# Performance work log

Hardware: AMD Instinct MI355X
Metric: run time of the kernel (lower is better)

Reference implementation:

```python
import jax, jax.numpy as jnp
import numpy as np

N_NODES = 100000
N_EDGES = 1600000
IN_DIM = 3
HID = 128


def setup_inputs() -> dict:
    key = jax.random.key(0)
    ks = jax.random.split(key, 16)
    s = 0.05
    inp = {
        "x": jax.random.normal(ks[0], (N_NODES, IN_DIM), dtype=jnp.float32),
        "pos": jax.random.normal(ks[1], (N_NODES, IN_DIM), dtype=jnp.float32),
        "edge_index": jax.random.randint(ks[2], (2, N_EDGES), 0, N_NODES, dtype=jnp.int64),
        # EdgeConv MLP: Linear(2*IN_DIM, HID) -> ReLU -> Linear(HID, HID)
        "w1": jax.random.normal(ks[3], (2 * IN_DIM, HID), dtype=jnp.float32) * s,
        "b1": jnp.zeros((HID,), dtype=jnp.float32),
        "w2": jax.random.normal(ks[4], (HID, HID), dtype=jnp.float32) * s,
        "b2": jnp.zeros((HID,), dtype=jnp.float32),
        # encoder tail: ReLU -> Linear(HID, HID)
        "w3": jax.random.normal(ks[5], (HID, HID), dtype=jnp.float32) * s,
        "b3": jnp.zeros((HID,), dtype=jnp.float32),
        # decoder: Linear(HID, HID) -> ReLU -> Linear(HID, 3)
        "w4": jax.random.normal(ks[6], (HID, HID), dtype=jnp.float32) * s,
        "b4": jnp.zeros((HID,), dtype=jnp.float32),
        "w5": jax.random.normal(ks[7], (HID, 3), dtype=jnp.float32) * s,
        "b5": jnp.zeros((3,), dtype=jnp.float32),
    }
    return inp


def reference(x, pos, edge_index, w1, b1, w2, b2, w3, b3, w4, b4, w5, b5):
    n = x.shape[0]
    src, dst = edge_index[0], edge_index[1]  # message j(src) -> i(dst)
    xi = x[dst]                               # [E, 3] target features
    xj = x[src]                               # [E, 3] source features
    msg_in = jnp.concatenate([xi, xj - xi], axis=-1)          # [E, 6]
    h = jax.nn.relu(msg_in @ w1 + b1) @ w2 + b2               # [E, HID]
    agg = jax.ops.segment_max(h, dst, num_segments=n)         # [N, HID]
    agg = jnp.where(jnp.isneginf(agg), 0.0, agg)              # nodes with no edges -> 0
    enc = jax.nn.relu(agg) @ w3 + b3                          # [N, HID]
    dec = jax.nn.relu(enc @ w4 + b4) @ w5 + b5                # [N, 3]
    return pos + 0.1 * jnp.tanh(dec)
```

## Files before the change

kernel.cpp:

```cpp
#include <hip/hip_runtime.h>
#include <hip/hip_bf16.h>

typedef __attribute__((ext_vector_type(8))) short short8;
typedef __attribute__((ext_vector_type(4))) float floatx4;
typedef __attribute__((ext_vector_type(2))) unsigned short ushortx2;

#define NHID 128
#define PADROW 136
#define EB 64
#define EB2 128
#define PB 256

__device__ __forceinline__ unsigned short f2bf(float x) {
  unsigned int u = __float_as_uint(x);
  u += 0x7FFFu + ((u >> 16) & 1u);
  return (unsigned short)(u >> 16);
}

__device__ __forceinline__ unsigned int pkbf(float a, float b) {
  __hip_bfloat162 h = __float22bfloat162_rn(make_float2(a, b));
  union { __hip_bfloat162 h; unsigned int u; } cv;
  cv.h = h;
  return cv.u;
}

__device__ __forceinline__ unsigned int pack2(float a, float b) {
  return (unsigned int)f2bf(a) | ((unsigned int)f2bf(b) << 16);
}

__device__ __forceinline__ unsigned int pkmax(unsigned int a, unsigned int b) {
  union { unsigned int u; ushortx2 v; } x, y;
  x.u = a; y.u = b;
  x.v = __builtin_elementwise_max(x.v, y.v);
  return x.u;
}

__device__ __forceinline__ void casmax(unsigned int* ap, unsigned int run) {
  unsigned int old = *ap;
  while (true) {
    unsigned int mx = pkmax(old, run);
    if (mx == old) break;
    unsigned int got = atomicCAS(ap, old, mx);
    if (got == old) break;
    old = got;
  }
}

__device__ __forceinline__ void load_bfrags(const float* __restrict__ wmat,
                                            short8* bf, int m, int q) {
  #pragma unroll
  for (int kc = 0; kc < 4; ++kc) {
    #pragma unroll
    for (int nt = 0; nt < 8; ++nt) {
      short8 v;
      #pragma unroll
      for (int j = 0; j < 8; ++j)
        v[j] = (short)f2bf(wmat[(kc * 32 + q * 8 + j) * NHID + nt * 16 + m]);
      bf[kc * 8 + nt] = v;
    }
  }
}

__device__ __forceinline__ void load_bfrags_perm(const float* __restrict__ wmat,
                                                 short8* bf, int m, int q) {
  #pragma unroll
  for (int kc = 0; kc < 4; ++kc) {
    #pragma unroll
    for (int nt = 0; nt < 8; ++nt) {
      short8 v;
      #pragma unroll
      for (int j = 0; j < 8; ++j) {
        const int khw = kc * 32 + q * 8 + j;
        const int ctrue = ((khw & 7) << 4) | (khw >> 3);
        v[j] = (short)f2bf(wmat[ctrue * NHID + nt * 16 + m]);
      }
      bf[kc * 8 + nt] = v;
    }
  }
}

__device__ __forceinline__ void mfma_block(const unsigned short* uA,
                                           const short8* bf, floatx4* acc,
                                           int w, int m, int q) {
  #pragma unroll
  for (int kc = 0; kc < 4; ++kc) {
    short8 a = *(const short8*)(uA + (16 * w + m) * PADROW + kc * 32 + q * 8);
    #pragma unroll
    for (int nt = 0; nt < 8; ++nt)
      acc[nt] = __builtin_amdgcn_mfma_f32_16x16x32_bf16(a, bf[kc * 8 + nt],
                                                        acc[nt], 0, 0, 0);
  }
}

__global__ void zero_detect_kernel(float4* __restrict__ p, int n4,
                                   const int* __restrict__ ei, int* __restrict__ flag) {
  if (blockIdx.x == 0 && threadIdx.x < 64) {
    unsigned long long b = __ballot(ei[2 * threadIdx.x + 1] != 0);
    if (threadIdx.x == 0) flag[0] = (b == 0ULL) ? 1 : 0;
  }
  int i = blockIdx.x * blockDim.x + threadIdx.x;
  int stride = gridDim.x * blockDim.x;
  float4 z = make_float4(0.f, 0.f, 0.f, 0.f);
  for (; i < n4; i += stride) p[i] = z;
}


__global__ __launch_bounds__(256) void part_hist(const int* __restrict__ ei,
                                                 const int* __restrict__ flag,
                                                 int* __restrict__ mat, int E, int nbuck) {
  __shared__ int hist[512];
  const bool is64 = flag[0] != 0;
  const int bl = blockIdx.x, t = threadIdx.x;
  for (int i = t; i < nbuck; i += 256) hist[i] = 0;
  __syncthreads();
  const int chunk = (E + PB - 1) / PB;
  const int lo = bl * chunk;
  const int hi = min(lo + chunk, E);
  for (int i = lo + t; i < hi; i += 256) {
    int d = is64 ? ei[2 * E + 2 * i] : ei[E + i];
    atomicAdd(&hist[d >> 8], 1);
  }
  __syncthreads();
  for (int bu = t; bu < nbuck; bu += 256) mat[bu * PB + bl] = hist[bu];
}

__global__ __launch_bounds__(256) void scan_rows(int* __restrict__ mat,
                                                 int* __restrict__ btot, int nbuck) {
  __shared__ int sh[256];
  const int bu = blockIdx.x, t = threadIdx.x;
  const int v = mat[bu * PB + t];
  sh[t] = v;
  __syncthreads();
  for (int off = 1; off < 256; off <<= 1) {
    int x = (t >= off) ? sh[t - off] : 0;
    __syncthreads();
    sh[t] += x;
    __syncthreads();
  }
  mat[bu * PB + t] = sh[t] - v;
  if (t == 255) btot[bu] = sh[255];
}

__global__ __launch_bounds__(512) void scan_buckets(const int* __restrict__ btot,
                                                    int* __restrict__ bstart, int nbuck) {
  __shared__ int sh[512];
  const int t = threadIdx.x;
  const int v = (t < nbuck) ? btot[t] : 0;
  sh[t] = v;
  __syncthreads();
  for (int off = 1; off < 512; off <<= 1) {
    int x = (t >= off) ? sh[t - off] : 0;
    __syncthreads();
    sh[t] += x;
    __syncthreads();
  }
  if (t <= nbuck) bstart[t] = sh[t] - v;
}

__global__ __launch_bounds__(256) void part_scatter(const int* __restrict__ ei,
                                                    const int* __restrict__ flag,
                                                    const int* __restrict__ mat,
                                                    const int* __restrict__ bstart,
                                                    int2* __restrict__ mid, int E, int nbuck) {
  __shared__ int off[512];
  const bool is64 = flag[0] != 0;
  const int bl = blockIdx.x, t = threadIdx.x;
  for (int bu = t; bu < nbuck; bu += 256) off[bu] = bstart[bu] + mat[bu * PB + bl];
  __syncthreads();
  const int chunk = (E + PB - 1) / PB;
  const int lo = bl * chunk;
  const int hi = min(lo + chunk, E);
  for (int i = lo + t; i < hi; i += 256) {
    int s = is64 ? ei[2 * i]         : ei[i];
    int d = is64 ? ei[2 * E + 2 * i] : ei[E + i];
    int p = atomicAdd(&off[d >> 8], 1);
    mid[p] = make_int2(s, d);
  }
}

__global__ __launch_bounds__(256) void bucket_sort(const int2* __restrict__ mid,
                                                   const int* __restrict__ bstart,
                                                   int2* __restrict__ sorted) {
  __shared__ int h[256], cnt[256];
  const int bu = blockIdx.x, t = threadIdx.x;
  const int lo = bstart[bu], hi = bstart[bu + 1];
  h[t] = 0; cnt[t] = 0;
  __syncthreads();
  for (int i = lo + t; i < hi; i += 256) atomicAdd(&h[mid[i].y & 255], 1);
  __syncthreads();
  const int v = h[t];
  for (int off = 1; off < 256; off <<= 1) {
    int x = (t >= off) ? h[t - off] : 0;
    __syncthreads();
    h[t] += x;
    __syncthreads();
  }
  const int excl = h[t] - v;
  __syncthreads();
  h[t] = excl;
  __syncthreads();
  for (int i = lo + t; i < hi; i += 256) {
    int2 e = mid[i];
    const int dl = e.y & 255;
    const int p = lo + h[dl] + atomicAdd(&cnt[dl], 1);
    sorted[p] = e;
  }
}


__global__ __launch_bounds__(512, 2) void edge_sorted_kernel(
    const float* __restrict__ x, const int2* __restrict__ sorted,
    const float* __restrict__ w1, const float* __restrict__ b1,
    const float* __restrict__ w2, const float* __restrict__ b2,
    unsigned int* aggu, int N, int E) {
  __shared__ unsigned short us[EB2 * PADROW];
  __shared__ short8 w2f[2048];
  __shared__ int esS[EB2], edS[EB2];
  __shared__ int pn[2];
  __shared__ unsigned long long maskS[2];

  const int t = threadIdx.x;
  const int lane = t & 63;
  const int w = t >> 6;
  const int m = lane & 15;
  const int q = lane >> 4;

  float b1c[8], b2c[8];
  #pragma unroll
  for (int nt = 0; nt < 8; ++nt) { b1c[nt] = b1[nt * 16 + m]; b2c[nt] = b2[nt * 16 + m]; }

  short8 bf1[8];
  #pragma unroll
  for (int nt = 0; nt < 8; ++nt) {
    short8 v;
    #pragma unroll
    for (int j = 0; j < 8; ++j)
      v[j] = (q == 0 && j < 6) ? (short)f2bf(w1[j * NHID + nt * 16 + m]) : (short)0;
    bf1[nt] = v;
  }

  for (int idx = t; idx < 2048; idx += 512) {
    const int fg = idx >> 6, ln = idx & 63;
    const int mm = ln & 15;
    const int kc = fg >> 3, nt = fg & 7;
    short8 v;
    #pragma unroll
    for (int j = 0; j < 8; ++j) {
      const int khw = kc * 32 + (ln >> 4) * 8 + j;
      const int ctrue = ((khw & 7) << 4) | (khw >> 3);
      v[j] = (short)f2bf(w2[ctrue * NHID + nt * 16 + mm]);
    }
    w2f[idx] = v;
  }

  const int jc = t & 63;
  const int quarter = t >> 6;

  const int nbt = (E + EB2 - 1) / EB2;
  __syncthreads();

  int2 sv = make_int2(0, -1);
  {
    const int tile0 = blockIdx.x;
    const int gb = tile0 * EB2;
    if (t < EB2) {
      const int e = gb + t;
      if (tile0 < nbt && e < E) sv = sorted[e];
    } else if (t == EB2) {
      sv.y = (tile0 < nbt && gb > 0) ? sorted[gb - 1].y : -2;
    } else if (t == EB2 + 1) {
      sv.y = (tile0 < nbt && gb + EB2 < E) ? sorted[gb + EB2].y : -2;
    }
  }

  for (int tile = blockIdx.x; tile < nbt; tile += gridDim.x) {
    if (t < EB2) { esS[t] = sv.x; edS[t] = sv.y; }
    else if (t == EB2) pn[0] = sv.y;
    else if (t == EB2 + 1) pn[1] = sv.y;
    __syncthreads();

    if (w == 0) {
      int d0 = edS[lane];
      int dp0 = (lane == 0) ? -9 : edS[lane - 1];
      unsigned long long mk0 = __ballot(lane == 0 || d0 != dp0);
      int d1 = edS[64 + lane];
      int dp1 = edS[63 + lane];
      unsigned long long mk1 = __ballot(d1 != dp1);
      if (lane == 0) { maskS[0] = mk0; maskS[1] = mk1; }
    }

    floatx4 acc[8];
    #pragma unroll
    for (int nt = 0; nt < 8; ++nt) { floatx4 z = {0.f, 0.f, 0.f, 0.f}; acc[nt] = z; }
    short8 a1 = {0, 0, 0, 0, 0, 0, 0, 0};
    if (q == 0) {
      const int e = 16 * w + m;
      const int si = esS[e];
      const int d0 = edS[e];
      const int di = (d0 < 0) ? 0 : d0;
      float xi0 = x[di * 3], xi1 = x[di * 3 + 1], xi2 = x[di * 3 + 2];
      float dd0 = x[si * 3] - xi0, dd1 = x[si * 3 + 1] - xi1, dd2 = x[si * 3 + 2] - xi2;
      union { short8 s; uint4 u; } cv;
      cv.u = make_uint4(pkbf(xi0, xi1), pkbf(xi2, dd0), pkbf(dd1, dd2), 0u);
      a1 = cv.s;
    }
    #pragma unroll
    for (int nt = 0; nt < 8; ++nt)
      acc[nt] = __builtin_amdgcn_mfma_f32_16x16x32_bf16(a1, bf1[nt], acc[nt], 0, 0, 0);

    #pragma unroll
    for (int r = 0; r < 4; ++r) {
      union { short8 s; uint4 u; } cv;
      cv.u = make_uint4(
        pkbf(fmaxf(acc[0][r] + b1c[0], 0.f), fmaxf(acc[1][r] + b1c[1], 0.f)),
        pkbf(fmaxf(acc[2][r] + b1c[2], 0.f), fmaxf(acc[3][r] + b1c[3], 0.f)),
        pkbf(fmaxf(acc[4][r] + b1c[4], 0.f), fmaxf(acc[5][r] + b1c[5], 0.f)),
        pkbf(fmaxf(acc[6][r] + b1c[6], 0.f), fmaxf(acc[7][r] + b1c[7], 0.f)));
      *(short8*)(&us[(16 * w + q * 4 + r) * PADROW + m * 8]) = cv.s;
    }
    __syncthreads();

    #pragma unroll
    for (int nt = 0; nt < 8; ++nt) { floatx4 z = {0.f, 0.f, 0.f, 0.f}; acc[nt] = z; }
    #pragma unroll
    for (int kc = 0; kc < 4; ++kc) {
      short8 a = *(const short8*)(&us[(16 * w + m) * PADROW + kc * 32 + q * 8]);
      #pragma unroll
      for (int nt = 0; nt < 8; ++nt)
        acc[nt] = __builtin_amdgcn_mfma_f32_16x16x32_bf16(a, w2f[(kc * 8 + nt) * 64 + lane],
                                                          acc[nt], 0, 0, 0);
    }
    __syncthreads();

    #pragma unroll
    for (int r = 0; r < 4; ++r) {
      union { short8 s; uint4 u; } cv;
      cv.u = make_uint4(
        pkbf(fmaxf(acc[0][r] + b2c[0], 0.f), fmaxf(acc[1][r] + b2c[1], 0.f)),
        pkbf(fmaxf(acc[2][r] + b2c[2], 0.f), fmaxf(acc[3][r] + b2c[3], 0.f)),
        pkbf(fmaxf(acc[4][r] + b2c[4], 0.f), fmaxf(acc[5][r] + b2c[5], 0.f)),
        pkbf(fmaxf(acc[6][r] + b2c[6], 0.f), fmaxf(acc[7][r] + b2c[7], 0.f)));
      *(short8*)(&us[(16 * w + q * 4 + r) * PADROW + m * 8]) = cv.s;
    }
    __syncthreads();

    {
      const int tn = tile + gridDim.x;
      const int gb = tn * EB2;
      int2 nv = make_int2(0, -1);
      if (t < EB2) {
        const int e = gb + t;
        if (tn < nbt && e < E) nv = sorted[e];
      } else if (t == EB2) {
        nv.y = (tn < nbt && gb > 0) ? sorted[gb - 1].y : -2;
      } else if (t == EB2 + 1) {
        nv.y = (tn < nbt && gb + EB2 < E) ? sorted[gb + EB2].y : -2;
      }
      sv = nv;
    }

    {
      const unsigned long long mk0 = maskS[0], mk1 = maskS[1];
      const int prevd = pn[0], nextd = pn[1];
      const int r0 = quarter * 16, r1 = r0 + 16;
      const unsigned int* us32 = (const unsigned int*)us;
      int s;
      if (r0 < 64) {
        s = 63 - __builtin_clzll(mk0 & (~0ULL >> (63 - r0)));
      } else {
        unsigned long long hm = mk1 & (~0ULL >> (127 - r0));
        s = hm ? 127 - __builtin_clzll(hm) : 63 - __builtin_clzll(mk0);
      }
      while (s < r1) {
        int nxt;
        if (s < 63) {
          unsigned long long ab = mk0 & (~0ULL << (s + 1));
          if (ab) nxt = __builtin_ffsll((long long)ab) - 1;
          else    nxt = mk1 ? 64 + __builtin_ffsll((long long)mk1) - 1 : 128;
        } else if (s == 63) {
          nxt = mk1 ? 64 + __builtin_ffsll((long long)mk1) - 1 : 128;
        } else if (s < 127) {
          unsigned long long ab = mk1 & (~0ULL << (s - 63));
          nxt = ab ? 64 + __builtin_ffsll((long long)ab) - 1 : 128;
        } else nxt = 128;

        const int d = edS[s];
        if (d >= 0) {
          const int lo = (s > r0) ? s : r0;
          const int hi = (nxt < r1) ? nxt : r1;
          unsigned int run = 0;
          for (int r = lo; r < hi; ++r)
            run = pkmax(run, us32[r * (PADROW >> 1) + jc]);
          const bool contained = (s >= r0) && (nxt <= r1);
          const bool bnd = (s == 0 && prevd == d) || (nxt == 128 && nextd == d);
          unsigned int* ap = aggu + (size_t)d * 64 + jc;
          if (contained && !bnd) *ap = run;
          else if (run) casmax(ap, run);
        }
        s = nxt;
      }
    }
    __syncthreads();
  }
}


__global__ __launch_bounds__(256, 2) void edge_atomic_kernel(
    const float* __restrict__ x, const int* __restrict__ ei,
    const float* __restrict__ w1, const float* __restrict__ b1,
    const float* __restrict__ w2, const float* __restrict__ b2,
    unsigned int* aggu, const int* __restrict__ flag64, int N, int E) {
  __shared__ unsigned short uA[EB * PADROW];
  __shared__ float w1s[6 * NHID];
  __shared__ float b1s[NHID], b2s[NHID];
  __shared__ int es[EB], ed[EB];

  const int t = threadIdx.x;
  const int lane = t & 63;
  const int w = t >> 6;
  const int m = lane & 15;
  const int q = lane >> 4;

  for (int i = t; i < 6 * NHID; i += 256) w1s[i] = w1[i];
  if (t < NHID) { b1s[t] = b1[t]; b2s[t] = b2[t]; }

  short8 bf[32];
  load_bfrags(w2, bf, m, q);

  const bool is64 = (flag64[0] != 0);
  const int nb = (E + EB - 1) / EB;

  for (int batch = blockIdx.x; batch < nb; batch += gridDim.x) {
    const int gbase = batch * EB;
    if (t < EB) {
      int e = gbase + t;
      es[t] = (e < E) ? (is64 ? ei[2 * e] : ei[e]) : 0;
    } else if (t < 2 * EB) {
      int tt = t - EB;
      int e = gbase + tt;
      ed[tt] = (e < E) ? (is64 ? ei[2 * E + 2 * e] : ei[E + e]) : 0;
    }
    __syncthreads();
    {
      const int e = t >> 2;
      const int c0 = (t & 3) * 32;
      const int si = es[e], di = ed[e];
      float xi0 = x[di * 3], xi1 = x[di * 3 + 1], xi2 = x[di * 3 + 2];
      float msg[6];
      msg[0] = xi0; msg[1] = xi1; msg[2] = xi2;
      msg[3] = x[si * 3] - xi0; msg[4] = x[si * 3 + 1] - xi1; msg[5] = x[si * 3 + 2] - xi2;
      unsigned int* d32 = (unsigned int*)uA;
      const int base32 = (e * PADROW + c0) >> 1;
      #pragma unroll
      for (int cc = 0; cc < 32; cc += 2) {
        float u0 = b1s[c0 + cc], u1 = b1s[c0 + cc + 1];
        #pragma unroll
        for (int d = 0; d < 6; ++d) {
          u0 += msg[d] * w1s[d * NHID + c0 + cc];
          u1 += msg[d] * w1s[d * NHID + c0 + cc + 1];
        }
        d32[base32 + (cc >> 1)] = pack2(fmaxf(u0, 0.f), fmaxf(u1, 0.f));
      }
    }
    __syncthreads();

    floatx4 acc[8];
    #pragma unroll
    for (int nt = 0; nt < 8; ++nt) { floatx4 z = {0.f, 0.f, 0.f, 0.f}; acc[nt] = z; }
    mfma_block(uA, bf, acc, w, m, q);

    #pragma unroll
    for (int nt = 0; nt < 8; ++nt) {
      const int c = nt * 16 + m;
      const float bb = b2s[c];
      const int kst = m * 8 + nt;
      #pragma unroll
      for (int r = 0; r < 4; ++r) {
        const int erow = 16 * w + q * 4 + r;
        if (gbase + erow < E) {
          float hb = acc[nt][r] + bb;
          if (hb > 0.f) {
            unsigned int v = (unsigned int)f2bf(hb);
            casmax(aggu + (size_t)ed[erow] * 64 + (kst >> 1), v << (16 * (kst & 1)));
          }
        }
      }
    }
    __syncthreads();
  }
}


__global__ __launch_bounds__(256, 2) void encdec_kernel(
    const float* __restrict__ w3, const float* __restrict__ b3,
    const float* __restrict__ w4, const float* __restrict__ b4,
    const float* __restrict__ w5, const float* __restrict__ b5,
    const float* __restrict__ pos, const unsigned short* __restrict__ agg16,
    float* __restrict__ out, int N) {
  __shared__ unsigned short uA[EB * PADROW];
  __shared__ short8 w4f[2048];
  __shared__ float w5s[NHID * 3];

  const int t = threadIdx.x;
  const int lane = t & 63;
  const int w = t >> 6;
  const int m = lane & 15;
  const int q = lane >> 4;

  float b3c[8], b4c[8];
  #pragma unroll
  for (int nt = 0; nt < 8; ++nt) { b3c[nt] = b3[nt * 16 + m]; b4c[nt] = b4[nt * 16 + m]; }

  short8 bf3[32];
  load_bfrags_perm(w3, bf3, m, q);

  for (int idx = t; idx < 2048; idx += 256) {
    const int fg = idx >> 6, ln = idx & 63;
    const int mm = ln & 15;
    const int kc = fg >> 3, nt = fg & 7;
    short8 v;
    #pragma unroll
    for (int j = 0; j < 8; ++j) {
      const int khw = kc * 32 + (ln >> 4) * 8 + j;
      const int ctrue = ((khw & 7) << 4) | (khw >> 3);
      v[j] = (short)f2bf(w4[ctrue * NHID + nt * 16 + mm]);
    }
    w4f[idx] = v;
  }
  for (int i = t; i < NHID * 3; i += 256) w5s[i] = w5[i];
  const float b50 = b5[0], b51 = b5[1], b52 = b5[2];

  const int ch = t & 15;
  const int rr = t >> 4;
  const int nb = (N + EB - 1) / EB;
  __syncthreads();

  uint4 rv[4];
  const uint4 uz = make_uint4(0u, 0u, 0u, 0u);
  {
    const int b0 = blockIdx.x;
    #pragma unroll
    for (int k = 0; k < 4; ++k) {
      const int node = b0 * EB + rr + 16 * k;
      rv[k] = (b0 < nb && node < N) ? ((const uint4*)agg16)[(size_t)node * 16 + ch] : uz;
    }
  }

  for (int batch = blockIdx.x; batch < nb; batch += gridDim.x) {
    const int base = batch * EB;
    #pragma unroll
    for (int k = 0; k < 4; ++k)
      *(uint4*)(&uA[(rr + 16 * k) * PADROW + ch * 8]) = rv[k];
    __syncthreads();

    {
      const int nxb = batch + gridDim.x;
      #pragma unroll
      for (int k = 0; k < 4; ++k) {
        const int node = nxb * EB + rr + 16 * k;
        rv[k] = (nxb < nb && node < N) ? ((const uint4*)agg16)[(size_t)node * 16 + ch] : uz;
      }
    }

    floatx4 acc[8];
    #pragma unroll
    for (int nt = 0; nt < 8; ++nt) { floatx4 z = {0.f, 0.f, 0.f, 0.f}; acc[nt] = z; }
    mfma_block(uA, bf3, acc, w, m, q);
    __syncthreads();

    #pragma unroll
    for (int r = 0; r < 4; ++r) {
      union { short8 s; uint4 u; } cv;
      cv.u = make_uint4(
        pkbf(acc[0][r] + b3c[0], acc[1][r] + b3c[1]),
        pkbf(acc[2][r] + b3c[2], acc[3][r] + b3c[3]),
        pkbf(acc[4][r] + b3c[4], acc[5][r] + b3c[5]),
        pkbf(acc[6][r] + b3c[6], acc[7][r] + b3c[7]));
      *(short8*)(&uA[(16 * w + q * 4 + r) * PADROW + m * 8]) = cv.s;
    }
    __syncthreads();

    #pragma unroll
    for (int nt = 0; nt < 8; ++nt) { floatx4 z = {0.f, 0.f, 0.f, 0.f}; acc[nt] = z; }
    #pragma unroll
    for (int kc = 0; kc < 4; ++kc) {
      short8 a = *(const short8*)(&uA[(16 * w + m) * PADROW + kc * 32 + q * 8]);
      #pragma unroll
      for (int nt = 0; nt < 8; ++nt)
        acc[nt] = __builtin_amdgcn_mfma_f32_16x16x32_bf16(a, w4f[(kc * 8 + nt) * 64 + lane],
                                                          acc[nt], 0, 0, 0);
    }

    float p[4][3];
    #pragma unroll
    for (int r = 0; r < 4; ++r) { p[r][0] = 0.f; p[r][1] = 0.f; p[r][2] = 0.f; }
    #pragma unroll
    for (int nt = 0; nt < 8; ++nt) {
      const int c = nt * 16 + m;
      const float bb = b4c[nt];
      const float w50 = w5s[c * 3], w51 = w5s[c * 3 + 1], w52 = w5s[c * 3 + 2];
      #pragma unroll
      for (int r = 0; r < 4; ++r) {
        float tv = fmaxf(acc[nt][r] + bb, 0.f);
        p[r][0] += tv * w50; p[r][1] += tv * w51; p[r][2] += tv * w52;
      }
    }
    #pragma unroll
    for (int off = 8; off >= 1; off >>= 1) {
      #pragma unroll
      for (int r = 0; r < 4; ++r) {
        p[r][0] += __shfl_xor(p[r][0], off, 16);
        p[r][1] += __shfl_xor(p[r][1], off, 16);
        p[r][2] += __shfl_xor(p[r][2], off, 16);
      }
    }
    if (m == 0) {
      #pragma unroll
      for (int r = 0; r < 4; ++r) {
        const int node = base + 16 * w + q * 4 + r;
        if (node < N) {
          out[node * 3]     = pos[node * 3]     + 0.1f * tanhf(p[r][0] + b50);
          out[node * 3 + 1] = pos[node * 3 + 1] + 0.1f * tanhf(p[r][1] + b51);
          out[node * 3 + 2] = pos[node * 3 + 2] + 0.1f * tanhf(p[r][2] + b52);
        }
      }
    }
    __syncthreads();
  }
}

extern "C" void kernel_launch(void* const* d_in, const int* in_sizes, int n_in,
                              void* d_out, int out_size, void* d_ws, size_t ws_size,
                              hipStream_t stream) {
  const float* x   = (const float*)d_in[0];
  const float* pos = (const float*)d_in[1];
  const int*   ei  = (const int*)d_in[2];
  const float* w1  = (const float*)d_in[3];
  const float* b1  = (const float*)d_in[4];
  const float* w2  = (const float*)d_in[5];
  const float* b2  = (const float*)d_in[6];
  const float* w3  = (const float*)d_in[7];
  const float* b3  = (const float*)d_in[8];
  const float* w4  = (const float*)d_in[9];
  const float* b4  = (const float*)d_in[10];
  const float* w5  = (const float*)d_in[11];
  const float* b5  = (const float*)d_in[12];
  float* out = (float*)d_out;

  const int N = in_sizes[0] / 3;
  const int E = in_sizes[2] / 2;
  const int nbuck = (N + 255) >> 8;

  char* ws = (char*)d_ws;
  unsigned short* agg16 = (unsigned short*)ws;
  const size_t aggB = (size_t)N * NHID * sizeof(unsigned short);
  int2* mid    = (int2*)(ws + aggB);
  int2* sorted = (int2*)(ws + aggB + (size_t)E * 8);
  int*  mat    = (int*)(ws + aggB + (size_t)E * 16);
  int*  btot   = mat + (size_t)nbuck * PB;
  int*  bstart = btot + nbuck;
  int*  flag   = bstart + nbuck + 2;
  const size_t needed = aggB + (size_t)E * 16 + ((size_t)nbuck * PB + 2 * nbuck + 8) * 4;

  if (ws_size >= needed && nbuck <= 511) {
    zero_detect_kernel<<<2048, 256, 0, stream>>>((float4*)agg16, N * 16, ei, flag);
    part_hist<<<PB, 256, 0, stream>>>(ei, flag, mat, E, nbuck);
    scan_rows<<<nbuck, 256, 0, stream>>>(mat, btot, nbuck);
    scan_buckets<<<1, 512, 0, stream>>>(btot, bstart, nbuck);
    part_scatter<<<PB, 256, 0, stream>>>(ei, flag, mat, bstart, mid, E, nbuck);
    bucket_sort<<<nbuck, 256, 0, stream>>>(mid, bstart, sorted);
    edge_sorted_kernel<<<512, 512, 0, stream>>>(x, sorted, w1, b1, w2, b2,
                                                (unsigned int*)agg16, N, E);
  } else {
    int* flag2 = (int*)(ws + aggB);
    zero_detect_kernel<<<2048, 256, 0, stream>>>((float4*)agg16, N * 16, ei, flag2);
    edge_atomic_kernel<<<512, 256, 0, stream>>>(x, ei, w1, b1, w2, b2,
                                                (unsigned int*)agg16, flag2, N, E);
  }
  encdec_kernel<<<512, 256, 0, stream>>>(w3, b3, w4, b4, w5, b5, pos, agg16, out, N);
}
```

Baseline: 360.2 us.

## Fuse zeroing into histogram kernel and combine cross-quarter segment maxima in shared memory

Drops the separate zero/detect kernel. The agg buffer is now zeroed by extra blocks of the histogram launch, and the int64 index format is detected inline in each kernel with a warp ballot. In the sorted edge kernel, segments that span several 16-row quarters are no longer each written with CAS atomics per quarter. Partial maxima go to a shared array and are merged by the quarter that owns the segment start, then written once. This removes a kernel launch and some global atomic traffic, at the cost of an extra barrier per tile and a redundant ballot load in each block.

```diff
diff --git a/kernel.cpp b/kernel.cpp
--- a/kernel.cpp
+++ b/kernel.cpp
@@ -46,6 +46,11 @@
   }
 }
 
+__device__ __forceinline__ bool detect64(const int* __restrict__ ei) {
+  unsigned long long b = __ballot(ei[2 * (threadIdx.x & 63) + 1] != 0);
+  return b == 0ULL;
+}
+
 __device__ __forceinline__ void load_bfrags(const float* __restrict__ wmat,
                                             short8* bf, int m, int q) {
   #pragma unroll
@@ -106,11 +111,18 @@
 
 
 __global__ __launch_bounds__(256) void part_hist(const int* __restrict__ ei,
-                                                 const int* __restrict__ flag,
-                                                 int* __restrict__ mat, int E, int nbuck) {
+                                                 int* __restrict__ mat, int E, int nbuck,
+                                                 float4* __restrict__ aggz, int n4) {
+  const int bl = blockIdx.x, t = threadIdx.x;
+  if (bl >= PB) {
+    int i = (bl - PB) * 256 + t;
+    const int st = (gridDim.x - PB) * 256;
+    float4 z = make_float4(0.f, 0.f, 0.f, 0.f);
+    for (; i < n4; i += st) aggz[i] = z;
+    return;
+  }
   __shared__ int hist[512];
-  const bool is64 = flag[0] != 0;
-  const int bl = blockIdx.x, t = threadIdx.x;
+  const bool is64 = detect64(ei);
   for (int i = t; i < nbuck; i += 256) hist[i] = 0;
   __syncthreads();
   const int chunk = (E + PB - 1) / PB;
@@ -158,12 +170,11 @@
 }
 
 __global__ __launch_bounds__(256) void part_scatter(const int* __restrict__ ei,
-                                                    const int* __restrict__ flag,
                                                     const int* __restrict__ mat,
                                                     const int* __restrict__ bstart,
                                                     int2* __restrict__ mid, int E, int nbuck) {
   __shared__ int off[512];
-  const bool is64 = flag[0] != 0;
+  const bool is64 = detect64(ei);
   const int bl = blockIdx.x, t = threadIdx.x;
   for (int bu = t; bu < nbuck; bu += 256) off[bu] = bstart[bu] + mat[bu * PB + bl];
   __syncthreads();
@@ -218,6 +229,7 @@
   __shared__ int esS[EB2], edS[EB2];
   __shared__ int pn[2];
   __shared__ unsigned long long maskS[2];
+  __shared__ unsigned int pmS[8][64];
 
   const int t = threadIdx.x;
   const int lane = t & 63;
@@ -359,6 +371,7 @@
       sv = nv;
     }
 
+    int os = -1, onxt = 0, od = -1; unsigned int opart = 0;
     {
       const unsigned long long mk0 = maskS[0], mk1 = maskS[1];
       const int prevd = pn[0], nextd = pn[1];
@@ -384,21 +397,39 @@
           nxt = ab ? 64 + __builtin_ffsll((long long)ab) - 1 : 128;
         } else nxt = 128;
 
-        const int d = edS[s];
-        if (d >= 0) {
-          const int lo = (s > r0) ? s : r0;
-          const int hi = (nxt < r1) ? nxt : r1;
-          unsigned int run = 0;
-          for (int r = lo; r < hi; ++r)
-            run = pkmax(run, us32[r * (PADROW >> 1) + jc]);
-          const bool contained = (s >= r0) && (nxt <= r1);
-          const bool bnd = (s == 0 && prevd == d) || (nxt == 128 && nextd == d);
-          unsigned int* ap = aggu + (size_t)d * 64 + jc;
-          if (contained && !bnd) *ap = run;
-          else if (run) casmax(ap, run);
+        const int lo = (s > r0) ? s : r0;
+        const int hi = (nxt < r1) ? nxt : r1;
+        unsigned int run = 0;
+        for (int r = lo; r < hi; ++r)
+          run = pkmax(run, us32[r * (PADROW >> 1) + jc]);
+
+        if (s < r0) {
+          pmS[quarter][jc] = run;
+        } else if (nxt <= r1) {
+          const int d = edS[s];
+          if (d >= 0) {
+            const bool bnd = (s == 0 && prevd == d) || (nxt == 128 && nextd == d);
+            unsigned int* ap = aggu + (size_t)d * 64 + jc;
+            if (!bnd) *ap = run;
+            else if (run) casmax(ap, run);
+          }
+        } else {
+          os = s; onxt = nxt; od = edS[s]; opart = run;
         }
         s = nxt;
       }
+    }
+    __syncthreads();
+
+    if (os >= 0 && od >= 0) {
+      const int endq = (onxt - 1) >> 4;
+      #pragma unroll 4
+      for (int qq = quarter + 1; qq <= endq; ++qq)
+        opart = pkmax(opart, pmS[qq][jc]);
+      const bool bnd = (os == 0 && pn[0] == od) || (onxt == 128 && pn[1] == od);
+      unsigned int* ap = aggu + (size_t)od * 64 + jc;
+      if (!bnd) *ap = opart;
+      else if (opart) casmax(ap, opart);
     }
     __syncthreads();
   }
@@ -662,12 +693,11 @@
   int*  flag   = bstart + nbuck + 2;
   const size_t needed = aggB + (size_t)E * 16 + ((size_t)nbuck * PB + 2 * nbuck + 8) * 4;
 
-  if (ws_size >= needed && nbuck <= 511) {
-    zero_detect_kernel<<<2048, 256, 0, stream>>>((float4*)agg16, N * 16, ei, flag);
-    part_hist<<<PB, 256, 0, stream>>>(ei, flag, mat, E, nbuck);
+  if (ws_size >= needed && nbuck <= 511 && E >= 64) {
+    part_hist<<<2048, 256, 0, stream>>>(ei, mat, E, nbuck, (float4*)agg16, N * 16);
     scan_rows<<<nbuck, 256, 0, stream>>>(mat, btot, nbuck);
     scan_buckets<<<1, 512, 0, stream>>>(btot, bstart, nbuck);
-    part_scatter<<<PB, 256, 0, stream>>>(ei, flag, mat, bstart, mid, E, nbuck);
+    part_scatter<<<PB, 256, 0, stream>>>(ei, mat, bstart, mid, E, nbuck);
     bucket_sort<<<nbuck, 256, 0, stream>>>(mid, bstart, sorted);
     edge_sorted_kernel<<<512, 512, 0, stream>>>(x, sorted, w1, b1, w2, b2,
                                                 (unsigned int*)agg16, N, E);
```

Result: no change. 354.2 us (-1.7%).
